# Kernel optimization log

Measured on AMD Instinct MI355X. Metric: run time of the kernel, lower is better.

The kernel has to match this reference:

```python
import jax, jax.numpy as jnp
import numpy as np

B, L, D = 32, 256, 512
D_STATE, D_CONV, EXPAND, NODE_DIM, D_FF = 16, 4, 2, 16, 2048
D_INNER = EXPAND * D
DT_RANK = D // 16


def _layernorm(x, g, b, eps=1e-5):
    mu = x.mean(-1, keepdims=True)
    var = ((x - mu) ** 2).mean(-1, keepdims=True)
    return (x - mu) * jax.lax.rsqrt(var + eps) * g + b


def _mamba(x, in_w, conv_w, conv_b, xproj_w, dt_w, dt_b, A_log, Dp, out_w):
    # Standard selective-scan (S6) Mamba inner block.
    Bb, Ll, _ = x.shape
    u, z = jnp.split(x @ in_w, 2, axis=-1)                # (B,L,d_inner) each
    pad = jnp.pad(u, ((0, 0), (D_CONV - 1, 0), (0, 0)))   # causal depthwise conv1d
    u = sum(pad[:, k:k + Ll, :] * conv_w[:, k] for k in range(D_CONV)) + conv_b
    u = jax.nn.silu(u)
    proj = u @ xproj_w                                    # (B,L,dt_rank+2*d_state)
    dt, Bm, Cm = jnp.split(proj, [DT_RANK, DT_RANK + D_STATE], axis=-1)
    dt = jax.nn.softplus(dt @ dt_w + dt_b)                # (B,L,d_inner)
    A = -jnp.exp(A_log)                                   # (d_inner,d_state)
    dA = jnp.exp(dt[..., None] * A)                       # (B,L,d_inner,d_state)
    dBu = dt[..., None] * Bm[:, :, None, :] * u[..., None]

    def step(h, inp):
        dA_t, dBu_t, C_t = inp
        h = dA_t * h + dBu_t
        return h, jnp.einsum('bds,bs->bd', h, C_t)

    h0 = jnp.zeros((Bb, D_INNER, D_STATE), x.dtype)
    _, ys = jax.lax.scan(step, h0, (dA.transpose(1, 0, 2, 3),
                                    dBu.transpose(1, 0, 2, 3),
                                    Cm.transpose(1, 0, 2)))
    y = ys.transpose(1, 0, 2) + u * Dp                    # (B,L,d_inner)
    return (y * jax.nn.silu(z)) @ out_w


def _forward(x,
             d_in_w, d_conv_w, d_conv_b, d_xproj_w, d_dt_w, d_dt_b, d_A_log, d_D, d_out_w, d_ln_g, d_ln_b,
             s_emb1, s_emb2, s_in_w, s_conv_w, s_conv_b, s_xproj_w, s_dt_w, s_dt_b, s_A_log, s_D, s_out_w, s_ln_g, s_ln_b,
             f_ln_g, f_ln_b, f_w1, f_b1, f_w2, f_b2):
    # DiffSSM: selective SSM on the first-differenced sequence, residual + LN
    xd = jnp.concatenate([x[:, :1], x[:, 1:] - x[:, :-1]], axis=1)
    x = _layernorm(x + _mamba(xd, d_in_w, d_conv_w, d_conv_b, d_xproj_w,
                              d_dt_w, d_dt_b, d_A_log, d_D, d_out_w),
                   d_ln_g, d_ln_b)
    # SpatialGraphMamba: learned adjacency over enc_in tokens, graph mix, SSM
    adj = jax.nn.softmax(jax.nn.relu(s_emb1 @ s_emb2.T), axis=-1)  # (enc_in,enc_in)
    xg = jnp.einsum('nl,bld->bnd', adj, x)
    x = _layernorm(x + _mamba(xg, s_in_w, s_conv_w, s_conv_b, s_xproj_w,
                              s_dt_w, s_dt_b, s_A_log, s_D, s_out_w),
                   s_ln_g, s_ln_b)
    # Pre-norm FFN with residual
    h = _layernorm(x, f_ln_g, f_ln_b)
    x = x + jax.nn.gelu(h @ f_w1 + f_b1) @ f_w2 + f_b2
    return x, adj


def setup_inputs() -> dict:
    key = jax.random.key(0)
    ks = iter(jax.random.split(key, 64))

    def rn(shape, s=0.02):
        return jax.random.normal(next(ks), shape, jnp.float32) * s

    A_log_init = jnp.log(jnp.broadcast_to(
        jnp.arange(1, D_STATE + 1, dtype=jnp.float32), (D_INNER, D_STATE)))
    dt_b_init = jnp.full((D_INNER,), -4.6, jnp.float32)  # softplus^-1(~0.01)

    inp = {'x': jax.random.normal(next(ks), (B, L, D), jnp.float32)}
    for p in ('d_', 's_'):
        inp[p + 'in_w'] = rn((D, 2 * D_INNER))
        inp[p + 'conv_w'] = rn((D_INNER, D_CONV), 0.1)
        inp[p + 'conv_b'] = jnp.zeros((D_INNER,), jnp.float32)
        inp[p + 'xproj_w'] = rn((D_INNER, DT_RANK + 2 * D_STATE))
        inp[p + 'dt_w'] = rn((DT_RANK, D_INNER))
        inp[p + 'dt_b'] = dt_b_init
        inp[p + 'A_log'] = A_log_init
        inp[p + 'D'] = jnp.ones((D_INNER,), jnp.float32)
        inp[p + 'out_w'] = rn((D_INNER, D))
        inp[p + 'ln_g'] = jnp.ones((D,), jnp.float32)
        inp[p + 'ln_b'] = jnp.zeros((D,), jnp.float32)
    inp['s_emb1'] = rn((L, NODE_DIM), 0.1)
    inp['s_emb2'] = rn((L, NODE_DIM), 0.1)
    inp['f_ln_g'] = jnp.ones((D,), jnp.float32)
    inp['f_ln_b'] = jnp.zeros((D,), jnp.float32)
    inp['f_w1'] = rn((D, D_FF))
    inp['f_b1'] = jnp.zeros((D_FF,), jnp.float32)
    inp['f_w2'] = rn((D_FF, D))
    inp['f_b2'] = jnp.zeros((D,), jnp.float32)
    return inp


def reference(x,
              d_in_w, d_conv_w, d_conv_b, d_xproj_w, d_dt_w, d_dt_b, d_A_log, d_D, d_out_w, d_ln_g, d_ln_b,
              s_emb1, s_emb2, s_in_w, s_conv_w, s_conv_b, s_xproj_w, s_dt_w, s_dt_b, s_A_log, s_D, s_out_w, s_ln_g, s_ln_b,
              f_ln_g, f_ln_b, f_w1, f_b1, f_w2, f_b2):
    return _forward(x,
                    d_in_w, d_conv_w, d_conv_b, d_xproj_w, d_dt_w, d_dt_b, d_A_log, d_D, d_out_w, d_ln_g, d_ln_b,
                    s_emb1, s_emb2, s_in_w, s_conv_w, s_conv_b, s_xproj_w, s_dt_w, s_dt_b, s_A_log, s_D, s_out_w, s_ln_g, s_ln_b,
                    f_ln_g, f_ln_b, f_w1, f_b1, f_w2, f_b2)
```

## Files before the change

### kernel.cpp

```cpp
#include <hip/hip_runtime.h>

#define DEV __device__ __forceinline__

typedef __bf16 bf16x8 __attribute__((ext_vector_type(8)));
typedef float  f32x4  __attribute__((ext_vector_type(4)));

DEV unsigned short f2b(float f) {
    union { float f; unsigned u; } v; v.f = f;
    unsigned r = v.u + 0x7fffu + ((v.u >> 16) & 1u);
    return (unsigned short)(r >> 16);
}
DEV float b2f(unsigned short h) {
    union { unsigned u; float f; } v; v.u = ((unsigned)h) << 16;
    return v.f;
}
DEV float sigmoidf_(float x) { return 1.f / (1.f + __expf(-x)); }
DEV float geluf_(float x) {
    float t = 0.7978845608028654f * (x + 0.044715f * x * x * x);
    return 0.5f * x * (1.f + tanhf(t));
}
DEV float softplusf_(float x) { return x > 15.f ? x : log1pf(__expf(x)); }
DEV void gload_lds16(const void* g, void* l) {
    __builtin_amdgcn_global_load_lds((const __attribute__((address_space(1))) void*)g,
                                     (__attribute__((address_space(3))) void*)l, 16, 0, 0);
}


struct WtDesc { const float* s; unsigned short* d; int K; int N; int t0; };
struct WtArgs { WtDesc m[12]; };

__global__ __launch_bounds__(256) void wtrans_k(WtArgs a) {
    __shared__ float tile[32][33];
    int t = blockIdx.x;
    int mi = 0;
#pragma unroll
    for (int j = 1; j < 12; j++) if (t >= a.m[j].t0) mi = j;
    const float* src0 = a.m[mi].s;
    unsigned short* dst0 = a.m[mi].d;
    const int K = a.m[mi].K, N = a.m[mi].N;
    const int lt = t - a.m[mi].t0;
    const int ntk = K >> 5;
    const int kt = lt % ntk, nt = lt / ntk;
    const int c = threadIdx.x & 31, r = threadIdx.x >> 5;
    const float* src = src0 + (size_t)(kt * 32) * N + nt * 32;
#pragma unroll
    for (int i = 0; i < 4; i++) tile[r + i * 8][c] = src[(size_t)(r + i * 8) * N + c];
    __syncthreads();
    unsigned short* dst = dst0 + (size_t)(nt * 32) * K + kt * 32;
#pragma unroll
    for (int i = 0; i < 4; i++) dst[(size_t)(r + i * 8) * K + c] = f2b(tile[c][r + i * 8]);
}

__global__ __launch_bounds__(256) void diff_k(const float* __restrict__ x,
                                              unsigned short* __restrict__ xd) {
    size_t i4 = (size_t)blockIdx.x * 256 + threadIdx.x;
    size_t idx = i4 * 4;
    int l = (int)((idx >> 9) & 255);
    float4 v = *(const float4*)&x[idx];
    if (l > 0) {
        float4 p = *(const float4*)&x[idx - 512];
        v.x -= p.x; v.y -= p.y; v.z -= p.z; v.w -= p.w;
    }
    unsigned short o[4] = {f2b(v.x), f2b(v.y), f2b(v.z), f2b(v.w)};
    *(unsigned long long*)&xd[idx] = *(unsigned long long*)o;
}

__global__ __launch_bounds__(256) void adj_k(const float* __restrict__ e1,
                                             const float* __restrict__ e2,
                                             float* __restrict__ adjf,
                                             unsigned short* __restrict__ adjb) {
    const int n = blockIdx.x, tid = threadIdx.x;
    __shared__ float e1s[16];
    __shared__ float redm[4], reds[4];
    if (tid < 16) e1s[tid] = e1[n * 16 + tid];
    __syncthreads();
    const float* e2r = e2 + tid * 16;
    float dot = 0.f;
#pragma unroll
    for (int k = 0; k < 16; k++) dot = fmaf(e1s[k], e2r[k], dot);
    float v = fmaxf(dot, 0.f);
    float m = v;
#pragma unroll
    for (int o = 32; o > 0; o >>= 1) m = fmaxf(m, __shfl_xor(m, o));
    const int lane = tid & 63, wv = tid >> 6;
    if (lane == 0) redm[wv] = m;
    __syncthreads();
    m = fmaxf(fmaxf(redm[0], redm[1]), fmaxf(redm[2], redm[3]));
    float e = __expf(v - m);
    float ssum = e;
#pragma unroll
    for (int o = 32; o > 0; o >>= 1) ssum += __shfl_xor(ssum, o);
    if (lane == 0) reds[wv] = ssum;
    __syncthreads();
    ssum = reds[0] + reds[1] + reds[2] + reds[3];
    float o = e / ssum;
    adjf[(size_t)n * 256 + tid] = o;
    adjb[(size_t)n * 256 + tid] = f2b(o);
}

template<int HBIAS, int HGELU>
__global__ __launch_bounds__(512, 2) void gemm256_k(
    const unsigned short* __restrict__ A, const unsigned short* __restrict__ Bt,
    unsigned short* __restrict__ C, const float* __restrict__ bias,
    int M, int N, int K, int lda) {
    constexpr int BM = 256, BN = 256, BK = 64;
    __shared__ __align__(16) unsigned short As[2][BM * BK];
    __shared__ __align__(16) unsigned short Bs[2][BN * BK];
    const int tid  = threadIdx.x;
    const int lane = tid & 63;
    const int wave = tid >> 6;
    const int wr = wave >> 2;
    const int wc = wave & 3;
    const int bm = blockIdx.x * BM, bn = blockIdx.y * BN;
    const int lrow  = lane & 15;
    const int klane = lane >> 4;

    f32x4 acc[8][4];
#pragma unroll
    for (int m = 0; m < 8; m++)
#pragma unroll
        for (int n = 0; n < 4; n++) {
            acc[m][n][0] = 0.f; acc[m][n][1] = 0.f; acc[m][n][2] = 0.f; acc[m][n][3] = 0.f;
        }

    auto STAGE = [&](int buf, int k0) {
#pragma unroll
        for (int it = 0; it < 4; ++it) {
            int flat = (it * 512 + tid) * 8;
            int r = flat >> 6, s = (flat & 63) >> 3;
            int c = (s ^ (r & 7)) * 8;
            gload_lds16(A + (size_t)(bm + r) * lda + (k0 + c),
                        &As[buf][(it * 512 + (tid & 448)) * 8]);
        }
#pragma unroll
        for (int it = 0; it < 4; ++it) {
            int flat = (it * 512 + tid) * 8;
            int r = flat >> 6, s = (flat & 63) >> 3;
            int c = (s ^ (r & 7)) * 8;
            gload_lds16(Bt + (size_t)(bn + r) * K + (k0 + c),
                        &Bs[buf][(it * 512 + (tid & 448)) * 8]);
        }
    };
    auto COMPUTE = [&](int buf) {
#pragma unroll
        for (int kk = 0; kk < 2; kk++) {
            bf16x8 af[8], bfv[4];
#pragma unroll
            for (int m = 0; m < 8; m++) {
                int rr = wr * 128 + m * 16 + lrow;
                int sl = (kk * 4 + klane) ^ (rr & 7);
                af[m] = *(const bf16x8*)&As[buf][rr * BK + sl * 8];
            }
#pragma unroll
            for (int n = 0; n < 4; n++) {
                int rr = wc * 64 + n * 16 + lrow;
                int sl = (kk * 4 + klane) ^ (rr & 7);
                bfv[n] = *(const bf16x8*)&Bs[buf][rr * BK + sl * 8];
            }
#pragma unroll
            for (int m = 0; m < 8; m++)
#pragma unroll
                for (int n = 0; n < 4; n++)
                    acc[m][n] = __builtin_amdgcn_mfma_f32_16x16x32_bf16(af[m], bfv[n], acc[m][n], 0, 0, 0);
        }
    };

    const int nt = K / BK;
    STAGE(0, 0);
    __syncthreads();
    for (int t = 0; t < nt; t += 2) {
        if (t + 1 < nt) STAGE(1, (t + 1) * BK);
        COMPUTE(0);
        __syncthreads();
        if (t + 1 < nt) {
            if (t + 2 < nt) STAGE(0, (t + 2) * BK);
            COMPUTE(1);
            if (t + 2 < nt) __syncthreads();
        }
    }

    const int r0 = (lane >> 4) << 2;
    unsigned short* Cs = As[0];
    constexpr int PITCH = BN + 8;
#pragma unroll
    for (int g = 0; g < 8; g++) {
        __syncthreads();
        if (wr == (g >> 2)) {
#pragma unroll
            for (int mm = 0; mm < 2; mm++) {
                const int m = (g & 3) * 2 + mm;
#pragma unroll
                for (int n = 0; n < 4; n++) {
                    const int cl = wc * 64 + n * 16 + lrow;
                    float bv = HBIAS ? bias[bn + cl] : 0.f;
#pragma unroll
                    for (int j = 0; j < 4; j++) {
                        float v = acc[m][n][j] + bv;
                        if (HGELU) v = geluf_(v);
                        Cs[(mm * 16 + r0 + j) * PITCH + cl] = f2b(v);
                    }
                }
            }
        }
        __syncthreads();
#pragma unroll
        for (int i = 0; i < 2; i++) {
            int flat = (i * 512 + tid) * 8;
            int row = flat >> 8, col = flat & 255;
            uint4 val = *(const uint4*)&Cs[row * PITCH + col];
            *(uint4*)&C[(size_t)(bm + g * 32 + row) * N + bn + col] = val;
        }
    }
}

template<int BM, int BN, int BK, int WRN, int FM, int FN,
         int OBF, int HBIAS, int HGELU, int HRES, int HSP>
__global__ __launch_bounds__(256) void gemm_k(
    const unsigned short* __restrict__ A, const unsigned short* __restrict__ Bt,
    void* __restrict__ C, const float* __restrict__ bias, const float* __restrict__ res,
    int M, int N, int K, int lda, long sA, long sB, long sC) {
    constexpr int SMASK = BK / 8 - 1;
    constexpr int KH    = BK / 32;
    __shared__ __align__(16) unsigned short As[BM * BK];
    __shared__ __align__(16) unsigned short Bs[BN * BK];
    const int tid  = threadIdx.x;
    const int lane = tid & 63;
    const int wave = tid >> 6;
    const int wr = wave / WRN, wc = wave % WRN;
    const int bm = blockIdx.x * BM, bn = blockIdx.y * BN;
    const unsigned short* Ab = A  + (size_t)blockIdx.z * sA;
    const unsigned short* Bb = Bt + (size_t)blockIdx.z * sB;
    const int lrow  = lane & 15;
    const int klane = lane >> 4;

    f32x4 acc[FM][FN];
#pragma unroll
    for (int m = 0; m < FM; m++)
#pragma unroll
        for (int n = 0; n < FN; n++) {
            acc[m][n][0] = 0.f; acc[m][n][1] = 0.f; acc[m][n][2] = 0.f; acc[m][n][3] = 0.f;
        }

    constexpr int AI = (BM * BK) / 2048;
    constexpr int BI = (BN * BK) / 2048;

    for (int k0 = 0; k0 < K; k0 += BK) {
#pragma unroll
        for (int it = 0; it < AI; ++it) {
            int flat = (it * 256 + tid) * 8;
            int r = flat / BK, s = (flat % BK) >> 3;
            int c = (s ^ (r & SMASK)) * 8;
            gload_lds16(Ab + (size_t)(bm + r) * lda + (k0 + c),
                        &As[(it * 256 + (tid & 192)) * 8]);
        }
#pragma unroll
        for (int it = 0; it < BI; ++it) {
            int flat = (it * 256 + tid) * 8;
            int r = flat / BK, s = (flat % BK) >> 3;
            int c = (s ^ (r & SMASK)) * 8;
            gload_lds16(Bb + (size_t)(bn + r) * K + (k0 + c),
                        &Bs[(it * 256 + (tid & 192)) * 8]);
        }
        __syncthreads();
#pragma unroll
        for (int kk = 0; kk < KH; kk++) {
            bf16x8 af[FM], bfv[FN];
#pragma unroll
            for (int m = 0; m < FM; m++) {
                int rr = wr * FM * 16 + m * 16 + lrow;
                int sl = (kk * 4 + klane) ^ (rr & SMASK);
                af[m] = *(const bf16x8*)&As[rr * BK + sl * 8];
            }
#pragma unroll
            for (int n = 0; n < FN; n++) {
                int rr = wc * FN * 16 + n * 16 + lrow;
                int sl = (kk * 4 + klane) ^ (rr & SMASK);
                bfv[n] = *(const bf16x8*)&Bs[rr * BK + sl * 8];
            }
#pragma unroll
            for (int m = 0; m < FM; m++)
#pragma unroll
                for (int n = 0; n < FN; n++)
                    acc[m][n] = __builtin_amdgcn_mfma_f32_16x16x32_bf16(af[m], bfv[n], acc[m][n], 0, 0, 0);
        }
        __syncthreads();
    }

    const int r0 = (lane >> 4) << 2;
    if (OBF) {
        unsigned short* Cs = Bs;
        constexpr int PITCH = BN + 8;
        unsigned short* Cg = (unsigned short*)C;
#pragma unroll
        for (int g = 0; g < BM / 32; g++) {
            __syncthreads();
            if (wr == (g * 2) / FM) {
                const int mb = (g * 2) % FM;
#pragma unroll
                for (int mm = 0; mm < 2; mm++) {
#pragma unroll
                    for (int n = 0; n < FN; n++) {
                        const int cl = wc * FN * 16 + n * 16 + lrow;
                        float bv = HBIAS ? bias[bn + cl] : 0.f;
#pragma unroll
                        for (int j = 0; j < 4; j++) {
                            float v = acc[mb + mm][n][j] + bv;
                            if (HSP)   v = softplusf_(v);
                            if (HGELU) v = geluf_(v);
                            Cs[(mm * 16 + r0 + j) * PITCH + cl] = f2b(v);
                        }
                    }
                }
            }
            __syncthreads();
#pragma unroll
            for (int i = 0; i < (32 * BN) / 2048; i++) {
                int flat = (i * 256 + tid) * 8;
                int row = flat / BN, col = flat % BN;
                uint4 val = *(const uint4*)&Cs[row * PITCH + col];
                size_t oi = (size_t)blockIdx.z * sC + (size_t)(bm + g * 32 + row) * N + bn + col;
                *(uint4*)&Cg[oi] = val;
            }
        }
    } else {
#pragma unroll
        for (int n = 0; n < FN; n++) {
            const int ccol = bn + wc * FN * 16 + n * 16 + lrow;
            float bv = HBIAS ? bias[ccol] : 0.f;
#pragma unroll
            for (int m = 0; m < FM; m++) {
#pragma unroll
                for (int j = 0; j < 4; j++) {
                    const int rrow = bm + wr * FM * 16 + m * 16 + r0 + j;
                    float v = acc[m][n][j] + bv;
                    if (HSP)   v = softplusf_(v);
                    if (HGELU) v = geluf_(v);
                    if (HRES)  v += res[(size_t)rrow * N + ccol];
                    ((float*)C)[(size_t)blockIdx.z * sC + (size_t)rrow * N + ccol] = v;
                }
            }
        }
    }
}

__global__ __launch_bounds__(256) void conv_k(const unsigned short* __restrict__ uz,
                                              const float* __restrict__ w,
                                              const float* __restrict__ cb,
                                              unsigned short* __restrict__ u) {
    int t = blockIdx.x * 256 + threadIdx.x;
    int dg = t & 127;
    size_t row = (size_t)(t >> 7);
    int l = (int)(row & 255);
    int d0 = dg * 8;
    float acc[8];
#pragma unroll
    for (int j = 0; j < 8; j++) acc[j] = cb[d0 + j];
#pragma unroll
    for (int k = 0; k < 4; k++) {
        int ls = l + k - 3;
        if (ls >= 0) {
            const unsigned short* src = uz + (((size_t)row + k - 3) << 11) + d0;
            uint4 v = *(const uint4*)src;
            const unsigned short* vs = (const unsigned short*)&v;
#pragma unroll
            for (int j = 0; j < 8; j++)
                acc[j] = fmaf(w[(d0 + j) * 4 + k], b2f(vs[j]), acc[j]);
        }
    }
    unsigned short o[8];
#pragma unroll
    for (int j = 0; j < 8; j++) {
        float a = acc[j];
        o[j] = f2b(a * sigmoidf_(a));
    }
    *(uint4*)(u + (row << 10) + d0) = *(const uint4*)o;
}

__global__ __launch_bounds__(256) void scan1_k(
    const float* __restrict__ dt,
    const unsigned short* __restrict__ u,
    const unsigned short* __restrict__ proj,
    const float* __restrict__ A_log,
    float* __restrict__ hend, float* __restrict__ Sc) {
    const int dg = blockIdx.x, c = blockIdx.y, b = blockIdx.z;
    const int d = dg * 256 + threadIdx.x;
    const size_t base = (size_t)b * 256 + c * 32;
    __shared__ float Bs[32][16];
    for (int i = threadIdx.x; i < 512; i += 256) {
        int r = i >> 4, s = i & 15;
        Bs[r][s] = b2f(proj[(base + r) * 64 + 32 + s]);
    }
    __syncthreads();
    float Aa[16];
#pragma unroll
    for (int s = 0; s < 16; s++) Aa[s] = -__expf(A_log[d * 16 + s]);
    float h[16];
#pragma unroll
    for (int s = 0; s < 16; s++) h[s] = 0.f;
    float ssum = 0.f;
    for (int l = 0; l < 32; l++) {
        size_t row = base + l;
        float dtv = dt[(row << 10) + d];
        float uu  = b2f(u[(row << 10) + d]);
        float du  = dtv * uu;
        ssum += dtv;
#pragma unroll
        for (int s = 0; s < 16; s++)
            h[s] = __expf(dtv * Aa[s]) * h[s] + du * Bs[l][s];
    }
    size_t o = (size_t)(b * 8 + c) * 1024 + d;
    Sc[o] = ssum;
#pragma unroll
    for (int s = 0; s < 16; s++) hend[o * 16 + s] = h[s];
}

__global__ __launch_bounds__(256) void scan2_k(
    const float* __restrict__ hend, const float* __restrict__ Sc,
    const float* __restrict__ A_log, float* __restrict__ hstart) {
    const int d = blockIdx.x * 256 + threadIdx.x;
    const int b = blockIdx.y;
    float Aa[16];
#pragma unroll
    for (int s = 0; s < 16; s++) Aa[s] = -__expf(A_log[d * 16 + s]);
    float h[16];
#pragma unroll
    for (int s = 0; s < 16; s++) h[s] = 0.f;
    for (int c = 0; c < 8; c++) {
        size_t o = (size_t)(b * 8 + c) * 1024 + d;
#pragma unroll
        for (int s = 0; s < 16; s++) hstart[o * 16 + s] = h[s];
        float sc = Sc[o];
#pragma unroll
        for (int s = 0; s < 16; s++)
            h[s] = __expf(sc * Aa[s]) * h[s] + hend[o * 16 + s];
    }
}

__global__ __launch_bounds__(256) void scan3_k(
    const float* __restrict__ dt,
    const unsigned short* __restrict__ u,
    const unsigned short* __restrict__ uz,
    const unsigned short* __restrict__ proj,
    const float* __restrict__ A_log,
    const float* __restrict__ Dp,
    const float* __restrict__ hstart,
    unsigned short* __restrict__ yg) {
    const int dg = blockIdx.x, c = blockIdx.y, b = blockIdx.z;
    const int d = dg * 256 + threadIdx.x;
    const size_t base = (size_t)b * 256 + c * 32;
    __shared__ float BCs[32][32];
    for (int i = threadIdx.x; i < 1024; i += 256) {
        int r = i >> 5, s = i & 31;
        BCs[r][s] = b2f(proj[(base + r) * 64 + 32 + s]);
    }
    __syncthreads();
    float Aa[16];
#pragma unroll
    for (int s = 0; s < 16; s++) Aa[s] = -__expf(A_log[d * 16 + s]);
    const float Dd = Dp[d];
    float h[16];
    size_t ho = ((size_t)(b * 8 + c) * 1024 + d) * 16;
#pragma unroll
    for (int s = 0; s < 16; s++) h[s] = hstart[ho + s];
    for (int l = 0; l < 32; l++) {
        size_t row = base + l;
        float dtv = dt[(row << 10) + d];
        float uu  = b2f(u[(row << 10) + d]);
        float zz  = b2f(uz[(row << 11) + 1024 + d]);
        float du  = dtv * uu;
        float y = 0.f;
#pragma unroll
        for (int s = 0; s < 16; s++) {
            h[s] = __expf(dtv * Aa[s]) * h[s] + du * BCs[l][s];
            y = fmaf(h[s], BCs[l][16 + s], y);
        }
        y = fmaf(uu, Dd, y);
        yg[(row << 10) + d] = f2b(y * (zz * sigmoidf_(zz)));
    }
}

template<int HRES, int OF32, int OBF>
__global__ __launch_bounds__(256) void ln_k(const float* __restrict__ xin,
                                            const float* __restrict__ resin,
                                            const float* __restrict__ g,
                                            const float* __restrict__ b,
                                            float* __restrict__ outf,
                                            unsigned short* __restrict__ outb) {
    const int row = blockIdx.x, tid = threadIdx.x;
    float2 v = ((const float2*)(xin + (size_t)row * 512))[tid];
    if (HRES) {
        float2 r2 = ((const float2*)(resin + (size_t)row * 512))[tid];
        v.x += r2.x; v.y += r2.y;
    }
    float s = v.x + v.y, q = v.x * v.x + v.y * v.y;
#pragma unroll
    for (int o = 32; o > 0; o >>= 1) { s += __shfl_xor(s, o); q += __shfl_xor(q, o); }
    __shared__ float sm[4], qm[4];
    const int lane = tid & 63, wv = tid >> 6;
    if (lane == 0) { sm[wv] = s; qm[wv] = q; }
    __syncthreads();
    s = sm[0] + sm[1] + sm[2] + sm[3];
    q = qm[0] + qm[1] + qm[2] + qm[3];
    const float mu = s * (1.f / 512.f);
    const float ri = rsqrtf(q * (1.f / 512.f) - mu * mu + 1e-5f);
    float2 gg = ((const float2*)g)[tid];
    float2 bb = ((const float2*)b)[tid];
    float o0 = (v.x - mu) * ri * gg.x + bb.x;
    float o1 = (v.y - mu) * ri * gg.y + bb.y;
    if (OF32) ((float2*)(outf + (size_t)row * 512))[tid] = make_float2(o0, o1);
    if (OBF) {
        unsigned short* ob = outb + (size_t)row * 512 + tid * 2;
        ob[0] = f2b(o0); ob[1] = f2b(o1);
    }
}

__global__ __launch_bounds__(256) void trans_k(const float* __restrict__ x1,
                                               unsigned short* __restrict__ xt) {
    __shared__ float tile[32][33];
    const int b = blockIdx.z;
    const int d0 = blockIdx.x * 32, l0 = blockIdx.y * 32;
    const int c = threadIdx.x & 31, r = threadIdx.x >> 5;
    const float* src = x1 + ((size_t)b * 256 + l0) * 512 + d0;
#pragma unroll
    for (int i = 0; i < 4; i++) tile[r + i * 8][c] = src[(size_t)(r + i * 8) * 512 + c];
    __syncthreads();
    unsigned short* dst = xt + ((size_t)b * 512 + d0) * 256 + l0;
#pragma unroll
    for (int i = 0; i < 4; i++) dst[(size_t)(r + i * 8) * 256 + c] = f2b(tile[c][r + i * 8]);
}

constexpr size_t OFF_WT_DIN  = 0;
constexpr size_t OFF_WT_SIN  = OFF_WT_DIN  + 2048ull * 512 * 2;
constexpr size_t OFF_WT_DOUT = OFF_WT_SIN  + 2048ull * 512 * 2;
constexpr size_t OFF_WT_SOUT = OFF_WT_DOUT + 512ull * 1024 * 2;
constexpr size_t OFF_WT_F1   = OFF_WT_SOUT + 512ull * 1024 * 2;
constexpr size_t OFF_WT_F2   = OFF_WT_F1   + 2048ull * 512 * 2;
constexpr size_t OFF_XPT_D   = OFF_WT_F2   + 512ull * 2048 * 2;
constexpr size_t OFF_XPT_S   = OFF_XPT_D   + 64ull * 1024 * 2;
constexpr size_t OFF_DTT_D   = OFF_XPT_S   + 64ull * 1024 * 2;
constexpr size_t OFF_DTT_S   = OFF_DTT_D   + 1024ull * 32 * 2;
constexpr size_t OFF_ACT     = OFF_DTT_S   + 1024ull * 32 * 2;
constexpr size_t OFF_UZ      = OFF_ACT  + 8192ull * 512 * 2;
constexpr size_t OFF_U       = OFF_UZ   + 8192ull * 2048 * 2;
constexpr size_t OFF_PROJ    = OFF_U    + 8192ull * 1024 * 2;
constexpr size_t OFF_YG      = OFF_PROJ + 8192ull * 64 * 2;
constexpr size_t OFF_MOUT    = OFF_YG   + 8192ull * 1024 * 2;
constexpr size_t OFF_X1      = OFF_MOUT + 8192ull * 512 * 4;
constexpr size_t OFF_X2      = OFF_X1   + 8192ull * 512 * 4;
constexpr size_t OFF_X1T     = OFF_X2   + 8192ull * 512 * 4;
constexpr size_t OFF_ADJB    = OFF_X1T  + 32ull * 512 * 256 * 2;
constexpr size_t OFF_DT      = OFF_ADJB + 256ull * 256 * 2;
constexpr size_t OFF_HST     = OFF_DT   + 8192ull * 1024 * 4;
constexpr size_t OFF_SC      = OFF_HST  + 32ull * 8 * 1024 * 16 * 4;

extern "C" void kernel_launch(void* const* d_in, const int* in_sizes, int n_in,
                              void* d_out, int out_size, void* d_ws, size_t ws_size,
                              hipStream_t stream) {
    (void)in_sizes; (void)n_in; (void)out_size; (void)ws_size;
    const float* x      = (const float*)d_in[0];
    const float* dinw   = (const float*)d_in[1];
    const float* dconvw = (const float*)d_in[2];
    const float* dconvb = (const float*)d_in[3];
    const float* dxproj = (const float*)d_in[4];
    const float* ddtw   = (const float*)d_in[5];
    const float* ddtb   = (const float*)d_in[6];
    const float* dAlog  = (const float*)d_in[7];
    const float* dD     = (const float*)d_in[8];
    const float* doutw  = (const float*)d_in[9];
    const float* dlng   = (const float*)d_in[10];
    const float* dlnb   = (const float*)d_in[11];
    const float* sinw   = (const float*)d_in[12];
    const float* sconvw = (const float*)d_in[13];
    const float* sconvb = (const float*)d_in[14];
    const float* sxproj = (const float*)d_in[15];
    const float* sdtw   = (const float*)d_in[16];
    const float* sdtb   = (const float*)d_in[17];
    const float* sAlog  = (const float*)d_in[18];
    const float* sD     = (const float*)d_in[19];
    const float* soutw  = (const float*)d_in[20];
    const float* slng   = (const float*)d_in[21];
    const float* slnb   = (const float*)d_in[22];
    const float* semb1  = (const float*)d_in[23];
    const float* semb2  = (const float*)d_in[24];
    const float* flng   = (const float*)d_in[25];
    const float* flnb   = (const float*)d_in[26];
    const float* fw1    = (const float*)d_in[27];
    const float* fb1    = (const float*)d_in[28];
    const float* fw2    = (const float*)d_in[29];
    const float* fb2    = (const float*)d_in[30];

    char* ws = (char*)d_ws;
    unsigned short* wtDin  = (unsigned short*)(ws + OFF_WT_DIN);
    unsigned short* wtSin  = (unsigned short*)(ws + OFF_WT_SIN);
    unsigned short* wtDout = (unsigned short*)(ws + OFF_WT_DOUT);
    unsigned short* wtSout = (unsigned short*)(ws + OFF_WT_SOUT);
    unsigned short* wtF1   = (unsigned short*)(ws + OFF_WT_F1);
    unsigned short* wtF2   = (unsigned short*)(ws + OFF_WT_F2);
    unsigned short* xptD   = (unsigned short*)(ws + OFF_XPT_D);
    unsigned short* xptS   = (unsigned short*)(ws + OFF_XPT_S);
    unsigned short* dttD   = (unsigned short*)(ws + OFF_DTT_D);
    unsigned short* dttS   = (unsigned short*)(ws + OFF_DTT_S);
    unsigned short* actIn  = (unsigned short*)(ws + OFF_ACT);
    unsigned short* uzBuf  = (unsigned short*)(ws + OFF_UZ);
    unsigned short* uBuf   = (unsigned short*)(ws + OFF_U);
    unsigned short* projB  = (unsigned short*)(ws + OFF_PROJ);
    unsigned short* ygBuf  = (unsigned short*)(ws + OFF_YG);
    float*          moutB  = (float*)(ws + OFF_MOUT);
    float*          hendB  = moutB;
    float*          x1Buf  = (float*)(ws + OFF_X1);
    float*          x2Buf  = (float*)(ws + OFF_X2);
    unsigned short* x1tBuf = (unsigned short*)(ws + OFF_X1T);
    unsigned short* adjB   = (unsigned short*)(ws + OFF_ADJB);
    float*          dtBuf  = (float*)(ws + OFF_DT);
    float*          hstB   = (float*)(ws + OFF_HST);
    float*          scB    = (float*)(ws + OFF_SC);
    unsigned short* hBuf   = uBuf;
    unsigned short* midBuf = uzBuf;

    float* outX   = (float*)d_out;
    float* outAdj = outX + 4194304;

    WtArgs wa;
    wa.m[0]  = WtDesc{dinw,   wtDin,  512,  2048, 0};
    wa.m[1]  = WtDesc{sinw,   wtSin,  512,  2048, 1024};
    wa.m[2]  = WtDesc{doutw,  wtDout, 1024, 512,  2048};
    wa.m[3]  = WtDesc{soutw,  wtSout, 1024, 512,  2560};
    wa.m[4]  = WtDesc{fw1,    wtF1,   512,  2048, 3072};
    wa.m[5]  = WtDesc{fw2,    wtF2,   2048, 512,  4096};
    wa.m[6]  = WtDesc{dxproj, xptD,   1024, 64,   5120};
    wa.m[7]  = WtDesc{sxproj, xptS,   1024, 64,   5184};
    wa.m[8]  = WtDesc{ddtw,   dttD,   32,   1024, 5248};
    wa.m[9]  = WtDesc{sdtw,   dttS,   32,   1024, 5280};
    wa.m[10] = WtDesc{dinw,   wtDin,  512,  2048, 0x7fffffff};
    wa.m[11] = WtDesc{dinw,   wtDin,  512,  2048, 0x7fffffff};
    wtrans_k<<<dim3(5312), dim3(256), 0, stream>>>(wa);

    diff_k<<<dim3(4096), dim3(256), 0, stream>>>(x, actIn);
    adj_k<<<dim3(256), dim3(256), 0, stream>>>(semb1, semb2, outAdj, adjB);

    gemm256_k<0,0><<<dim3(32,8), dim3(512), 0, stream>>>(
        actIn, wtDin, uzBuf, nullptr, 8192, 2048, 512, 512);
    conv_k<<<dim3(4096), dim3(256), 0, stream>>>(uzBuf, dconvw, dconvb, uBuf);
    gemm_k<64,64,64,2,2,2, 1,0,0,0,0><<<dim3(128,1,1), dim3(256), 0, stream>>>(
        uBuf, xptD, projB, nullptr, nullptr, 8192, 64, 1024, 1024, 0, 0, 0);
    gemm_k<128,128,32,2,4,4, 0,1,0,0,1><<<dim3(64,8,1), dim3(256), 0, stream>>>(
        projB, dttD, dtBuf, ddtb, nullptr, 8192, 1024, 32, 64, 0, 0, 0);
    scan1_k<<<dim3(4,8,32), dim3(256), 0, stream>>>(dtBuf, uBuf, projB, dAlog, hendB, scB);
    scan2_k<<<dim3(4,32),   dim3(256), 0, stream>>>(hendB, scB, dAlog, hstB);
    scan3_k<<<dim3(4,8,32), dim3(256), 0, stream>>>(dtBuf, uBuf, uzBuf, projB, dAlog, dD, hstB, ygBuf);
    gemm_k<128,128,64,2,4,4, 0,0,0,0,0><<<dim3(64,4,1), dim3(256), 0, stream>>>(
        ygBuf, wtDout, moutB, nullptr, nullptr, 8192, 512, 1024, 1024, 0, 0, 0);
    ln_k<1,1,0><<<dim3(8192), dim3(256), 0, stream>>>(moutB, x, dlng, dlnb, x1Buf, nullptr);

    trans_k<<<dim3(16,8,32), dim3(256), 0, stream>>>(x1Buf, x1tBuf);
    gemm_k<128,128,64,2,4,4, 1,0,0,0,0><<<dim3(2,4,32), dim3(256), 0, stream>>>(
        adjB, x1tBuf, actIn, nullptr, nullptr, 256, 512, 256, 256, 0, 131072, 131072);
    gemm256_k<0,0><<<dim3(32,8), dim3(512), 0, stream>>>(
        actIn, wtSin, uzBuf, nullptr, 8192, 2048, 512, 512);
    conv_k<<<dim3(4096), dim3(256), 0, stream>>>(uzBuf, sconvw, sconvb, uBuf);
    gemm_k<64,64,64,2,2,2, 1,0,0,0,0><<<dim3(128,1,1), dim3(256), 0, stream>>>(
        uBuf, xptS, projB, nullptr, nullptr, 8192, 64, 1024, 1024, 0, 0, 0);
    gemm_k<128,128,32,2,4,4, 0,1,0,0,1><<<dim3(64,8,1), dim3(256), 0, stream>>>(
        projB, dttS, dtBuf, sdtb, nullptr, 8192, 1024, 32, 64, 0, 0, 0);
    scan1_k<<<dim3(4,8,32), dim3(256), 0, stream>>>(dtBuf, uBuf, projB, sAlog, hendB, scB);
    scan2_k<<<dim3(4,32),   dim3(256), 0, stream>>>(hendB, scB, sAlog, hstB);
    scan3_k<<<dim3(4,8,32), dim3(256), 0, stream>>>(dtBuf, uBuf, uzBuf, projB, sAlog, sD, hstB, ygBuf);
    gemm_k<128,128,64,2,4,4, 0,0,0,0,0><<<dim3(64,4,1), dim3(256), 0, stream>>>(
        ygBuf, wtSout, moutB, nullptr, nullptr, 8192, 512, 1024, 1024, 0, 0, 0);
    ln_k<1,1,0><<<dim3(8192), dim3(256), 0, stream>>>(moutB, x1Buf, slng, slnb, x2Buf, nullptr);

    ln_k<0,0,1><<<dim3(8192), dim3(256), 0, stream>>>(x2Buf, nullptr, flng, flnb, nullptr, hBuf);
    gemm256_k<1,1><<<dim3(32,8), dim3(512), 0, stream>>>(
        hBuf, wtF1, midBuf, fb1, 8192, 2048, 512, 512);
    gemm_k<128,128,64,2,4,4, 0,1,0,1,0><<<dim3(64,4,1), dim3(256), 0, stream>>>(
        midBuf, wtF2, outX, fb2, x2Buf, 8192, 512, 2048, 2048, 0, 0, 0);
}
```

Before: 637.7 us.

## Double-buffer GEMM K-loop with vmcnt waits and store dt as bf16

Both GEMM kernels switch to a two-stage LDS pipeline: two tiles are prefetched, and each iteration waits with s_waitcnt vmcnt for only the older tile before a raw barrier. This lets global-to-LDS loads overlap MFMA compute instead of fully draining each step. The generic gemm_k now uses double LDS buffers, which doubles its shared memory and may lower occupancy. Separately, the dt projection output is written in bf16 instead of fp32 to halve traffic into the scan kernels, at some precision cost.

```diff
diff --git a/kernel.cpp b/kernel.cpp
--- a/kernel.cpp
+++ b/kernel.cpp
@@ -23,6 +23,9 @@
 DEV void gload_lds16(const void* g, void* l) {
     __builtin_amdgcn_global_load_lds((const __attribute__((address_space(1))) void*)g,
                                      (__attribute__((address_space(3))) void*)l, 16, 0, 0);
+}
+template<int N> DEV void waitv() {
+    asm volatile("s_waitcnt vmcnt(%0)" :: "n"(N) : "memory");
 }
 
 
@@ -104,6 +107,7 @@
     unsigned short* __restrict__ C, const float* __restrict__ bias,
     int M, int N, int K, int lda) {
     constexpr int BM = 256, BN = 256, BK = 64;
+    constexpr int STN = 8;
     __shared__ __align__(16) unsigned short As[2][BM * BK];
     __shared__ __align__(16) unsigned short Bs[2][BN * BK];
     const int tid  = threadIdx.x;
@@ -167,16 +171,13 @@
 
     const int nt = K / BK;
     STAGE(0, 0);
-    __syncthreads();
-    for (int t = 0; t < nt; t += 2) {
-        if (t + 1 < nt) STAGE(1, (t + 1) * BK);
-        COMPUTE(0);
-        __syncthreads();
-        if (t + 1 < nt) {
-            if (t + 2 < nt) STAGE(0, (t + 2) * BK);
-            COMPUTE(1);
-            if (t + 2 < nt) __syncthreads();
-        }
+    if (nt > 1) STAGE(1, BK);
+    for (int t = 0; t < nt; ++t) {
+        if (t + 1 < nt) waitv<STN>(); else waitv<0>();
+        __builtin_amdgcn_s_barrier();
+        COMPUTE(t & 1);
+        __builtin_amdgcn_s_barrier();
+        if (t + 2 < nt) STAGE(t & 1, (t + 2) * BK);
     }
 
     const int r0 = (lane >> 4) << 2;
@@ -221,8 +222,11 @@
     int M, int N, int K, int lda, long sA, long sB, long sC) {
     constexpr int SMASK = BK / 8 - 1;
     constexpr int KH    = BK / 32;
-    __shared__ __align__(16) unsigned short As[BM * BK];
-    __shared__ __align__(16) unsigned short Bs[BN * BK];
+    constexpr int AI = (BM * BK) / 2048;
+    constexpr int BI = (BN * BK) / 2048;
+    constexpr int STN = AI + BI;
+    __shared__ __align__(16) unsigned short As[2][BM * BK];
+    __shared__ __align__(16) unsigned short Bs[2][BN * BK];
     const int tid  = threadIdx.x;
     const int lane = tid & 63;
     const int wave = tid >> 6;
@@ -241,17 +245,14 @@
             acc[m][n][0] = 0.f; acc[m][n][1] = 0.f; acc[m][n][2] = 0.f; acc[m][n][3] = 0.f;
         }
 
-    constexpr int AI = (BM * BK) / 2048;
-    constexpr int BI = (BN * BK) / 2048;
-
-    for (int k0 = 0; k0 < K; k0 += BK) {
+    auto STAGE = [&](int buf, int k0) {
 #pragma unroll
         for (int it = 0; it < AI; ++it) {
             int flat = (it * 256 + tid) * 8;
             int r = flat / BK, s = (flat % BK) >> 3;
             int c = (s ^ (r & SMASK)) * 8;
             gload_lds16(Ab + (size_t)(bm + r) * lda + (k0 + c),
-                        &As[(it * 256 + (tid & 192)) * 8]);
+                        &As[buf][(it * 256 + (tid & 192)) * 8]);
         }
 #pragma unroll
         for (int it = 0; it < BI; ++it) {
@@ -259,9 +260,10 @@
             int r = flat / BK, s = (flat % BK) >> 3;
             int c = (s ^ (r & SMASK)) * 8;
             gload_lds16(Bb + (size_t)(bn + r) * K + (k0 + c),
-                        &Bs[(it * 256 + (tid & 192)) * 8]);
-        }
-        __syncthreads();
+                        &Bs[buf][(it * 256 + (tid & 192)) * 8]);
+        }
+    };
+    auto COMPUTE = [&](int buf) {
 #pragma unroll
         for (int kk = 0; kk < KH; kk++) {
             bf16x8 af[FM], bfv[FN];
@@ -269,13 +271,13 @@
             for (int m = 0; m < FM; m++) {
                 int rr = wr * FM * 16 + m * 16 + lrow;
                 int sl = (kk * 4 + klane) ^ (rr & SMASK);
-                af[m] = *(const bf16x8*)&As[rr * BK + sl * 8];
+                af[m] = *(const bf16x8*)&As[buf][rr * BK + sl * 8];
             }
 #pragma unroll
             for (int n = 0; n < FN; n++) {
                 int rr = wc * FN * 16 + n * 16 + lrow;
                 int sl = (kk * 4 + klane) ^ (rr & SMASK);
-                bfv[n] = *(const bf16x8*)&Bs[rr * BK + sl * 8];
+                bfv[n] = *(const bf16x8*)&Bs[buf][rr * BK + sl * 8];
             }
 #pragma unroll
             for (int m = 0; m < FM; m++)
@@ -283,12 +285,22 @@
                 for (int n = 0; n < FN; n++)
                     acc[m][n] = __builtin_amdgcn_mfma_f32_16x16x32_bf16(af[m], bfv[n], acc[m][n], 0, 0, 0);
         }
-        __syncthreads();
+    };
+
+    const int nt = K / BK;
+    STAGE(0, 0);
+    if (nt > 1) STAGE(1, BK);
+    for (int t = 0; t < nt; ++t) {
+        if (t + 1 < nt) waitv<STN>(); else waitv<0>();
+        __builtin_amdgcn_s_barrier();
+        COMPUTE(t & 1);
+        __builtin_amdgcn_s_barrier();
+        if (t + 2 < nt) STAGE(t & 1, (t + 2) * BK);
     }
 
     const int r0 = (lane >> 4) << 2;
     if (OBF) {
-        unsigned short* Cs = Bs;
+        unsigned short* Cs = Bs[0];
         constexpr int PITCH = BN + 8;
         unsigned short* Cg = (unsigned short*)C;
 #pragma unroll
@@ -377,7 +389,7 @@
 }
 
 __global__ __launch_bounds__(256) void scan1_k(
-    const float* __restrict__ dt,
+    const unsigned short* __restrict__ dt,
     const unsigned short* __restrict__ u,
     const unsigned short* __restrict__ proj,
     const float* __restrict__ A_log,
@@ -400,7 +412,7 @@
     float ssum = 0.f;
     for (int l = 0; l < 32; l++) {
         size_t row = base + l;
-        float dtv = dt[(row << 10) + d];
+        float dtv = b2f(dt[(row << 10) + d]);
         float uu  = b2f(u[(row << 10) + d]);
         float du  = dtv * uu;
         ssum += dtv;
@@ -437,7 +449,7 @@
 }
 
 __global__ __launch_bounds__(256) void scan3_k(
-    const float* __restrict__ dt,
+    const unsigned short* __restrict__ dt,
     const unsigned short* __restrict__ u,
     const unsigned short* __restrict__ uz,
     const unsigned short* __restrict__ proj,
@@ -464,7 +476,7 @@
     for (int s = 0; s < 16; s++) h[s] = hstart[ho + s];
     for (int l = 0; l < 32; l++) {
         size_t row = base + l;
-        float dtv = dt[(row << 10) + d];
+        float dtv = b2f(dt[(row << 10) + d]);
         float uu  = b2f(u[(row << 10) + d]);
         float zz  = b2f(uz[(row << 11) + 1024 + d]);
         float du  = dtv * uu;
@@ -550,7 +562,7 @@
 constexpr size_t OFF_X1T     = OFF_X2   + 8192ull * 512 * 4;
 constexpr size_t OFF_ADJB    = OFF_X1T  + 32ull * 512 * 256 * 2;
 constexpr size_t OFF_DT      = OFF_ADJB + 256ull * 256 * 2;
-constexpr size_t OFF_HST     = OFF_DT   + 8192ull * 1024 * 4;
+constexpr size_t OFF_HST     = OFF_DT   + 8192ull * 1024 * 2;
 constexpr size_t OFF_SC      = OFF_HST  + 32ull * 8 * 1024 * 16 * 4;
 
 extern "C" void kernel_launch(void* const* d_in, const int* in_sizes, int n_in,
@@ -611,7 +623,7 @@
     float*          x2Buf  = (float*)(ws + OFF_X2);
     unsigned short* x1tBuf = (unsigned short*)(ws + OFF_X1T);
     unsigned short* adjB   = (unsigned short*)(ws + OFF_ADJB);
-    float*          dtBuf  = (float*)(ws + OFF_DT);
+    unsigned short* dtBuf  = (unsigned short*)(ws + OFF_DT);
     float*          hstB   = (float*)(ws + OFF_HST);
     float*          scB    = (float*)(ws + OFF_SC);
     unsigned short* hBuf   = uBuf;
@@ -643,7 +655,7 @@
     conv_k<<<dim3(4096), dim3(256), 0, stream>>>(uzBuf, dconvw, dconvb, uBuf);
     gemm_k<64,64,64,2,2,2, 1,0,0,0,0><<<dim3(128,1,1), dim3(256), 0, stream>>>(
         uBuf, xptD, projB, nullptr, nullptr, 8192, 64, 1024, 1024, 0, 0, 0);
-    gemm_k<128,128,32,2,4,4, 0,1,0,0,1><<<dim3(64,8,1), dim3(256), 0, stream>>>(
+    gemm_k<128,128,32,2,4,4, 1,1,0,0,1><<<dim3(64,8,1), dim3(256), 0, stream>>>(
         projB, dttD, dtBuf, ddtb, nullptr, 8192, 1024, 32, 64, 0, 0, 0);
     scan1_k<<<dim3(4,8,32), dim3(256), 0, stream>>>(dtBuf, uBuf, projB, dAlog, hendB, scB);
     scan2_k<<<dim3(4,32),   dim3(256), 0, stream>>>(hendB, scB, dAlog, hstB);
@@ -660,7 +672,7 @@
     conv_k<<<dim3(4096), dim3(256), 0, stream>>>(uzBuf, sconvw, sconvb, uBuf);
     gemm_k<64,64,64,2,2,2, 1,0,0,0,0><<<dim3(128,1,1), dim3(256), 0, stream>>>(
         uBuf, xptS, projB, nullptr, nullptr, 8192, 64, 1024, 1024, 0, 0, 0);
-    gemm_k<128,128,32,2,4,4, 0,1,0,0,1><<<dim3(64,8,1), dim3(256), 0, stream>>>(
+    gemm_k<128,128,32,2,4,4, 1,1,0,0,1><<<dim3(64,8,1), dim3(256), 0, stream>>>(
         projB, dttS, dtBuf, sdtb, nullptr, 8192, 1024, 32, 64, 0, 0, 0);
     scan1_k<<<dim3(4,8,32), dim3(256), 0, stream>>>(dtBuf, uBuf, projB, sAlog, hendB, scB);
     scan2_k<<<dim3(4,32),   dim3(256), 0, stream>>>(hendB, scB, sAlog, hstB);
```

Result: slower. 671.9 us (+5.4%).

## Fuse dt projection and softplus into scan kernels; swizzle gemm256 block order

Applied to the files above, without the earlier changes.

Removes the separate dt GEMM, which wrote an 8192x1024 fp32 dt buffer that was then read by both scan passes. Each scan thread now keeps its 32 dt_proj weights in registers, stages the dt-rank columns of proj in LDS, and computes dt with 32 FMAs plus softplus per step. This adds redundant compute (scan1 and scan3 both recompute dt) and register pressure in exchange for removing a large memory round trip and two launches. Separately, the 256x256 GEMM remaps block IDs so that consecutive workgroups land in the same group of eight, which is intended to improve cache locality across XCDs.

```diff
diff --git a/kernel.cpp b/kernel.cpp
--- a/kernel.cpp
+++ b/kernel.cpp
@@ -111,7 +111,12 @@
     const int wave = tid >> 6;
     const int wr = wave >> 2;
     const int wc = wave & 3;
-    const int bm = blockIdx.x * BM, bn = blockIdx.y * BN;
+    const int nwgx = gridDim.x;
+    const int nwg  = nwgx * gridDim.y;
+    const int id   = blockIdx.y * nwgx + blockIdx.x;
+    const int cpx  = nwg >> 3;
+    const int sw   = (id & 7) * cpx + (id >> 3);
+    const int bm = (sw % nwgx) * BM, bn = (sw / nwgx) * BN;
     const int lrow  = lane & 15;
     const int klane = lane >> 4;
 
@@ -377,20 +382,30 @@
 }
 
 __global__ __launch_bounds__(256) void scan1_k(
-    const float* __restrict__ dt,
+    const unsigned short* __restrict__ proj,
     const unsigned short* __restrict__ u,
-    const unsigned short* __restrict__ proj,
+    const float* __restrict__ dtw,
+    const float* __restrict__ dtb,
     const float* __restrict__ A_log,
     float* __restrict__ hend, float* __restrict__ Sc) {
     const int dg = blockIdx.x, c = blockIdx.y, b = blockIdx.z;
     const int d = dg * 256 + threadIdx.x;
     const size_t base = (size_t)b * 256 + c * 32;
     __shared__ float Bs[32][16];
+    __shared__ float Pd[32][32];
     for (int i = threadIdx.x; i < 512; i += 256) {
         int r = i >> 4, s = i & 15;
         Bs[r][s] = b2f(proj[(base + r) * 64 + 32 + s]);
     }
-    __syncthreads();
+    for (int i = threadIdx.x; i < 1024; i += 256) {
+        int r = i >> 5, s = i & 31;
+        Pd[r][s] = b2f(proj[(base + r) * 64 + s]);
+    }
+    __syncthreads();
+    float w[32];
+#pragma unroll
+    for (int r = 0; r < 32; r++) w[r] = dtw[r * 1024 + d];
+    const float dtbv = dtb[d];
     float Aa[16];
 #pragma unroll
     for (int s = 0; s < 16; s++) Aa[s] = -__expf(A_log[d * 16 + s]);
@@ -400,7 +415,10 @@
     float ssum = 0.f;
     for (int l = 0; l < 32; l++) {
         size_t row = base + l;
-        float dtv = dt[(row << 10) + d];
+        float dtr = dtbv;
+#pragma unroll
+        for (int r = 0; r < 32; r++) dtr = fmaf(w[r], Pd[l][r], dtr);
+        const float dtv = softplusf_(dtr);
         float uu  = b2f(u[(row << 10) + d]);
         float du  = dtv * uu;
         ssum += dtv;
@@ -437,10 +455,11 @@
 }
 
 __global__ __launch_bounds__(256) void scan3_k(
-    const float* __restrict__ dt,
+    const unsigned short* __restrict__ proj,
     const unsigned short* __restrict__ u,
     const unsigned short* __restrict__ uz,
-    const unsigned short* __restrict__ proj,
+    const float* __restrict__ dtw,
+    const float* __restrict__ dtb,
     const float* __restrict__ A_log,
     const float* __restrict__ Dp,
     const float* __restrict__ hstart,
@@ -449,11 +468,17 @@
     const int d = dg * 256 + threadIdx.x;
     const size_t base = (size_t)b * 256 + c * 32;
     __shared__ float BCs[32][32];
+    __shared__ float Pd[32][32];
     for (int i = threadIdx.x; i < 1024; i += 256) {
         int r = i >> 5, s = i & 31;
         BCs[r][s] = b2f(proj[(base + r) * 64 + 32 + s]);
-    }
-    __syncthreads();
+        Pd[r][s]  = b2f(proj[(base + r) * 64 + s]);
+    }
+    __syncthreads();
+    float w[32];
+#pragma unroll
+    for (int r = 0; r < 32; r++) w[r] = dtw[r * 1024 + d];
+    const float dtbv = dtb[d];
     float Aa[16];
 #pragma unroll
     for (int s = 0; s < 16; s++) Aa[s] = -__expf(A_log[d * 16 + s]);
@@ -464,7 +489,10 @@
     for (int s = 0; s < 16; s++) h[s] = hstart[ho + s];
     for (int l = 0; l < 32; l++) {
         size_t row = base + l;
-        float dtv = dt[(row << 10) + d];
+        float dtr = dtbv;
+#pragma unroll
+        for (int r = 0; r < 32; r++) dtr = fmaf(w[r], Pd[l][r], dtr);
+        const float dtv = softplusf_(dtr);
         float uu  = b2f(u[(row << 10) + d]);
         float zz  = b2f(uz[(row << 11) + 1024 + d]);
         float du  = dtv * uu;
@@ -537,9 +565,7 @@
 constexpr size_t OFF_WT_F2   = OFF_WT_F1   + 2048ull * 512 * 2;
 constexpr size_t OFF_XPT_D   = OFF_WT_F2   + 512ull * 2048 * 2;
 constexpr size_t OFF_XPT_S   = OFF_XPT_D   + 64ull * 1024 * 2;
-constexpr size_t OFF_DTT_D   = OFF_XPT_S   + 64ull * 1024 * 2;
-constexpr size_t OFF_DTT_S   = OFF_DTT_D   + 1024ull * 32 * 2;
-constexpr size_t OFF_ACT     = OFF_DTT_S   + 1024ull * 32 * 2;
+constexpr size_t OFF_ACT     = OFF_XPT_S   + 64ull * 1024 * 2;
 constexpr size_t OFF_UZ      = OFF_ACT  + 8192ull * 512 * 2;
 constexpr size_t OFF_U       = OFF_UZ   + 8192ull * 2048 * 2;
 constexpr size_t OFF_PROJ    = OFF_U    + 8192ull * 1024 * 2;
@@ -549,8 +575,7 @@
 constexpr size_t OFF_X2      = OFF_X1   + 8192ull * 512 * 4;
 constexpr size_t OFF_X1T     = OFF_X2   + 8192ull * 512 * 4;
 constexpr size_t OFF_ADJB    = OFF_X1T  + 32ull * 512 * 256 * 2;
-constexpr size_t OFF_DT      = OFF_ADJB + 256ull * 256 * 2;
-constexpr size_t OFF_HST     = OFF_DT   + 8192ull * 1024 * 4;
+constexpr size_t OFF_HST     = OFF_ADJB + 256ull * 256 * 2;
 constexpr size_t OFF_SC      = OFF_HST  + 32ull * 8 * 1024 * 16 * 4;
 
 extern "C" void kernel_launch(void* const* d_in, const int* in_sizes, int n_in,
@@ -598,8 +623,6 @@
     unsigned short* wtF2   = (unsigned short*)(ws + OFF_WT_F2);
     unsigned short* xptD   = (unsigned short*)(ws + OFF_XPT_D);
     unsigned short* xptS   = (unsigned short*)(ws + OFF_XPT_S);
-    unsigned short* dttD   = (unsigned short*)(ws + OFF_DTT_D);
-    unsigned short* dttS   = (unsigned short*)(ws + OFF_DTT_S);
     unsigned short* actIn  = (unsigned short*)(ws + OFF_ACT);
     unsigned short* uzBuf  = (unsigned short*)(ws + OFF_UZ);
     unsigned short* uBuf   = (unsigned short*)(ws + OFF_U);
@@ -611,7 +634,6 @@
     float*          x2Buf  = (float*)(ws + OFF_X2);
     unsigned short* x1tBuf = (unsigned short*)(ws + OFF_X1T);
     unsigned short* adjB   = (unsigned short*)(ws + OFF_ADJB);
-    float*          dtBuf  = (float*)(ws + OFF_DT);
     float*          hstB   = (float*)(ws + OFF_HST);
     float*          scB    = (float*)(ws + OFF_SC);
     unsigned short* hBuf   = uBuf;
@@ -629,11 +651,11 @@
     wa.m[5]  = WtDesc{fw2,    wtF2,   2048, 512,  4096};
     wa.m[6]  = WtDesc{dxproj, xptD,   1024, 64,   5120};
     wa.m[7]  = WtDesc{sxproj, xptS,   1024, 64,   5184};
-    wa.m[8]  = WtDesc{ddtw,   dttD,   32,   1024, 5248};
-    wa.m[9]  = WtDesc{sdtw,   dttS,   32,   1024, 5280};
+    wa.m[8]  = WtDesc{dinw,   wtDin,  512,  2048, 0x7fffffff};
+    wa.m[9]  = WtDesc{dinw,   wtDin,  512,  2048, 0x7fffffff};
     wa.m[10] = WtDesc{dinw,   wtDin,  512,  2048, 0x7fffffff};
     wa.m[11] = WtDesc{dinw,   wtDin,  512,  2048, 0x7fffffff};
-    wtrans_k<<<dim3(5312), dim3(256), 0, stream>>>(wa);
+    wtrans_k<<<dim3(5248), dim3(256), 0, stream>>>(wa);
 
     diff_k<<<dim3(4096), dim3(256), 0, stream>>>(x, actIn);
     adj_k<<<dim3(256), dim3(256), 0, stream>>>(semb1, semb2, outAdj, adjB);
@@ -643,11 +665,9 @@
     conv_k<<<dim3(4096), dim3(256), 0, stream>>>(uzBuf, dconvw, dconvb, uBuf);
     gemm_k<64,64,64,2,2,2, 1,0,0,0,0><<<dim3(128,1,1), dim3(256), 0, stream>>>(
         uBuf, xptD, projB, nullptr, nullptr, 8192, 64, 1024, 1024, 0, 0, 0);
-    gemm_k<128,128,32,2,4,4, 0,1,0,0,1><<<dim3(64,8,1), dim3(256), 0, stream>>>(
-        projB, dttD, dtBuf, ddtb, nullptr, 8192, 1024, 32, 64, 0, 0, 0);
-    scan1_k<<<dim3(4,8,32), dim3(256), 0, stream>>>(dtBuf, uBuf, projB, dAlog, hendB, scB);
+    scan1_k<<<dim3(4,8,32), dim3(256), 0, stream>>>(projB, uBuf, ddtw, ddtb, dAlog, hendB, scB);
     scan2_k<<<dim3(4,32),   dim3(256), 0, stream>>>(hendB, scB, dAlog, hstB);
-    scan3_k<<<dim3(4,8,32), dim3(256), 0, stream>>>(dtBuf, uBuf, uzBuf, projB, dAlog, dD, hstB, ygBuf);
+    scan3_k<<<dim3(4,8,32), dim3(256), 0, stream>>>(projB, uBuf, uzBuf, ddtw, ddtb, dAlog, dD, hstB, ygBuf);
     gemm_k<128,128,64,2,4,4, 0,0,0,0,0><<<dim3(64,4,1), dim3(256), 0, stream>>>(
         ygBuf, wtDout, moutB, nullptr, nullptr, 8192, 512, 1024, 1024, 0, 0, 0);
     ln_k<1,1,0><<<dim3(8192), dim3(256), 0, stream>>>(moutB, x, dlng, dlnb, x1Buf, nullptr);
@@ -660,11 +680,9 @@
     conv_k<<<dim3(4096), dim3(256), 0, stream>>>(uzBuf, sconvw, sconvb, uBuf);
     gemm_k<64,64,64,2,2,2, 1,0,0,0,0><<<dim3(128,1,1), dim3(256), 0, stream>>>(
         uBuf, xptS, projB, nullptr, nullptr, 8192, 64, 1024, 1024, 0, 0, 0);
-    gemm_k<128,128,32,2,4,4, 0,1,0,0,1><<<dim3(64,8,1), dim3(256), 0, stream>>>(
-        projB, dttS, dtBuf, sdtb, nullptr, 8192, 1024, 32, 64, 0, 0, 0);
-    scan1_k<<<dim3(4,8,32), dim3(256), 0, stream>>>(dtBuf, uBuf, projB, sAlog, hendB, scB);
+    scan1_k<<<dim3(4,8,32), dim3(256), 0, stream>>>(projB, uBuf, sdtw, sdtb, sAlog, hendB, scB);
     scan2_k<<<dim3(4,32),   dim3(256), 0, stream>>>(hendB, scB, sAlog, hstB);
-    scan3_k<<<dim3(4,8,32), dim3(256), 0, stream>>>(dtBuf, uBuf, uzBuf, projB, sAlog, sD, hstB, ygBuf);
+    scan3_k<<<dim3(4,8,32), dim3(256), 0, stream>>>(projB, uBuf, uzBuf, sdtw, sdtb, sAlog, sD, hstB, ygBuf);
     gemm_k<128,128,64,2,4,4, 0,0,0,0,0><<<dim3(64,4,1), dim3(256), 0, stream>>>(
         ygBuf, wtSout, moutB, nullptr, nullptr, 8192, 512, 1024, 1024, 0, 0, 0);
     ln_k<1,1,0><<<dim3(8192), dim3(256), 0, stream>>>(moutB, x1Buf, slng, slnb, x2Buf, nullptr);
```

Measured after the change: 697.5 us. +9.4%, slower.
